# Kernel tuning notes

Hardware: AMD Instinct MI355X
Metric: run time of the kernel (lower is better)

Reference implementation:

```python
import jax, jax.numpy as jnp
import numpy as np

NTOKENS = 8192   # max_ntokens
TOPK = 2
H = 1024         # hidden
FFN = 4096       # ffn_hidden = 4*hidden
E = 8            # nexperts
M = NTOKENS * TOPK          # total dispatched rows (flux_m_max)
CAP = M // E                # balanced rows per expert


def setup_inputs() -> dict:
    key = jax.random.key(0)
    k1, k2, k3, k4 = jax.random.split(key, 4)
    x = jax.random.normal(k1, (NTOKENS, H), jnp.float32)
    weight0 = jax.random.normal(k2, (E, H, FFN), jnp.float32) * 0.02
    weight1 = jax.random.normal(k3, (E, FFN, H), jnp.float32) * 0.02
    # Balanced routing: scatter_index[t, k] is the row in the expert-sorted
    # dispatched buffer; a permutation of arange(M) gives exactly CAP rows/expert.
    scatter_index = jax.random.permutation(k4, M).reshape(NTOKENS, TOPK).astype(jnp.int32)
    splits = jnp.full((E,), CAP, dtype=jnp.int32)  # rows per expert, sum == M
    return {"x": x, "weight0": weight0, "weight1": weight1,
            "scatter_index": scatter_index, "splits": splits}


def reference(x, weight0, weight1, scatter_index, splits):
    ntokens, topk = scatter_index.shape
    n_exp, h, ffn = weight0.shape
    m = ntokens * topk
    cap = m // n_exp  # splits are balanced by construction (== splits[e])
    # --- AG-scatter: place each (token, k) replica at its dispatched row ---
    vals = jnp.repeat(x, topk, axis=0)                              # [M, h]
    dispatched = jnp.zeros((m, h), x.dtype).at[scatter_index.reshape(-1)].set(vals)
    xe = dispatched.reshape(n_exp, cap, h)                          # [E, C, h]
    # --- grouped GEMM 0 + exact GELU (torch F.gelu default = erf form) ---
    mid = jax.nn.gelu(jnp.einsum('ech,ehf->ecf', xe, weight0), approximate=False)
    # --- grouped GEMM 1 ---
    ye = jnp.einsum('ecf,efh->ech', mid, weight1).reshape(m, h)     # [M, h]
    # --- gather-RS: combine topk expert outputs per token ---
    return ye[scatter_index].sum(axis=1)                            # [ntokens, h]
```

## Files before the change

kernel.cpp:

```cpp
#include <hip/hip_runtime.h>
#include <hip/hip_bf16.h>
#include <cstdint>

constexpr int NT   = 8192;
constexpr int H    = 1024;
constexpr int FFN  = 4096;
constexpr int E    = 8;
constexpr int M    = NT * 2;
constexpr int CAP  = M / E;

typedef unsigned short u16;
typedef short short8 __attribute__((ext_vector_type(8)));
typedef float f32x4 __attribute__((ext_vector_type(4)));

__device__ int g_inv[M];

__device__ __forceinline__ u16 f2bf(float f) {
  union { float f; unsigned u; } c{f};
  unsigned r = (c.u + 0x7FFFu + ((c.u >> 16) & 1u)) >> 16;
  return (u16)r;
}
__device__ __forceinline__ void async16(const void* g, void* l) {
  auto gp = reinterpret_cast<const __attribute__((address_space(1))) unsigned*>(
      reinterpret_cast<uintptr_t>(g));
  auto lp = reinterpret_cast<__attribute__((address_space(3))) unsigned*>(
      reinterpret_cast<uintptr_t>(l));
  __builtin_amdgcn_global_load_lds(gp, lp, 16, 0, 0);
}

__device__ __forceinline__ void transpose_body(const float* __restrict__ W,
                                               u16* __restrict__ WT,
                                               int K, int N, int tb,
                                               void* smem_) {
  float (*tile)[65] = (float(*)[65])smem_;
  const int ntx = N >> 6;
  const int per = ntx * (K >> 6);
  const int e   = tb / per;
  const int rem = tb - e * per;
  const int bx  = rem % ntx;
  const int by  = rem / ntx;
  const float* Wp = W + (size_t)e * K * N;
  u16* Tp = WT + (size_t)e * K * N;
  const int k0 = by * 64, n0 = bx * 64;
  const int tid = threadIdx.x;

  const int u = tid & 15, krb = tid >> 4;
#pragma unroll
  for (int p = 0; p < 4; ++p) {
    const int kr = p * 16 + krb;
    float4 v = *(const float4*)&Wp[(size_t)(k0 + kr) * N + n0 + u * 4];
    tile[kr][u * 4 + 0] = v.x;
    tile[kr][u * 4 + 1] = v.y;
    tile[kr][u * 4 + 2] = v.z;
    tile[kr][u * 4 + 3] = v.w;
  }
  __syncthreads();

  const int n = tid >> 3, cb = tid & 7;
#pragma unroll
  for (int p = 0; p < 2; ++p) {
    const int nn = p * 32 + n;
    u16 pack[8];
#pragma unroll
    for (int j = 0; j < 8; ++j) pack[j] = f2bf(tile[cb * 8 + j][nn]);
    *(short8*)&Tp[(size_t)(n0 + nn) * K + k0 + cb * 8] = *(short8*)pack;
  }
}

__global__ __launch_bounds__(256)
void pre_kernel(const float* __restrict__ x, const float* __restrict__ w0,
                const int* __restrict__ sidx, u16* __restrict__ wt0,
                u16* __restrict__ disp, float* __restrict__ outz) {
  __shared__ float tile[64][65];
  const int b = blockIdx.x;
  const int tid = threadIdx.x;
  if (b < 8192) {
    transpose_body(w0, wt0, H, FFN, b, tile);
    return;
  }
  if (b < 16384) {
    const int t = b - 8192;
    const int r0 = sidx[2 * t + 0];
    const int r1 = sidx[2 * t + 1];
    float4 v = ((const float4*)(x + (size_t)t * H))[tid];
    ushort4 bb;
    bb.x = f2bf(v.x); bb.y = f2bf(v.y); bb.z = f2bf(v.z); bb.w = f2bf(v.w);
    ((ushort4*)disp)[(size_t)r0 * (H / 4) + tid] = bb;
    ((ushort4*)disp)[(size_t)r1 * (H / 4) + tid] = bb;
    return;
  }
  if (b < 16448) {
    const int i = (b - 16384) * 256 + tid;
    g_inv[sidx[i]] = i >> 1;
    return;
  }
  const int zb = b - 16448;
  float4 z = {0.f, 0.f, 0.f, 0.f};
#pragma unroll
  for (int p = 0; p < 4; ++p)
    ((float4*)outz)[(size_t)zb * 1024 + p * 256 + tid] = z;
}

template <bool GELU, bool ATOMIC>
__global__ __launch_bounds__(256)
void gemm_bt_kernel(const u16* __restrict__ A,
                    const u16* __restrict__ Bt,
                    u16* __restrict__ C,
                    float* __restrict__ outp,
                    int Mn, int Nn, int Kn, int ny,
                    const float* __restrict__ Wx, u16* __restrict__ WTx,
                    int Kx, int Nx) {
  __shared__ __align__(16) char smem[32768];
  int b = blockIdx.x;
  if (Wx != nullptr) {
    const int g = b / 3, r = b - g * 3;
    if (r != 0) { transpose_body(Wx, WTx, Kx, Nx, g * 2 + (r - 1), smem); return; }
    b = g;
  }
  u16* lA = (u16*)smem;
  u16* lB = (u16*)(smem + 16384);

  const int e = b & 7;
  const int t = b >> 3;
  const int q = t & 15, s = t >> 4;
  const int sy = ny >> 2;
  const int sm = s % sy, sn = s / sy;
  const int tm = sm * 4 + (q & 3), tn = sn * 4 + (q >> 2);
  const int m0 = tm * 128, n0 = tn * 128;

  const u16* Ae = A  + (size_t)e * Mn * Kn + (size_t)m0 * Kn;
  const u16* Be = Bt + (size_t)e * Nn * Kn + (size_t)n0 * Kn;

  const int tid  = threadIdx.x;
  const int lane = tid & 63;
  const int wave = tid >> 6;
  const int wr = wave >> 1, wc = wave & 1;
  const int lhi = lane >> 4, llo = lane & 15;

  const int sr = lane >> 3;
  const int gc = (lane & 7) ^ sr;

  f32x4 acc[4][4] = {};

  for (int kt = 0; kt < Kn; kt += 64) {
#pragma unroll
    for (int s2 = 0; s2 < 4; ++s2) {
      const int i = wave * 4 + s2;
      const int row = i * 8 + sr;
      async16(Ae + (size_t)row * Kn + kt + gc * 8, &lA[i * 512]);
      async16(Be + (size_t)row * Kn + kt + gc * 8, &lB[i * 512]);
    }
    __syncthreads();

#pragma unroll
    for (int ks = 0; ks < 2; ++ks) {
      short8 af[4], bf[4];
#pragma unroll
      for (int i = 0; i < 4; ++i) {
        const int row = wr * 64 + i * 16 + llo;
        const int pc = (ks * 4 + lhi) ^ (llo & 7);
        af[i] = *(const short8*)&lA[row * 64 + pc * 8];
      }
#pragma unroll
      for (int j = 0; j < 4; ++j) {
        const int row = wc * 64 + j * 16 + llo;
        const int pc = (ks * 4 + lhi) ^ (llo & 7);
        bf[j] = *(const short8*)&lB[row * 64 + pc * 8];
      }
#pragma unroll
      for (int i = 0; i < 4; ++i)
#pragma unroll
        for (int j = 0; j < 4; ++j)
          acc[i][j] = __builtin_amdgcn_mfma_f32_16x16x32_bf16(af[i], bf[j], acc[i][j], 0, 0, 0);
    }
    __syncthreads();
  }

  if (!ATOMIC) {
    u16* Ce = C + (size_t)e * Mn * Nn;
#pragma unroll
    for (int i = 0; i < 4; ++i) {
      const int mrow = m0 + wr * 64 + i * 16 + lhi * 4;
#pragma unroll
      for (int j = 0; j < 4; ++j) {
        const int ncol = n0 + wc * 64 + j * 16 + llo;
#pragma unroll
        for (int r = 0; r < 4; ++r) {
          float v = acc[i][j][r];
          if (GELU) v = 0.5f * v * (1.0f + erff(v * 0.70710678118654752f));
          Ce[(size_t)(mrow + r) * Nn + ncol] = f2bf(v);
        }
      }
    }
  } else {
    const int grBase = e * Mn + m0 + wr * 64;
#pragma unroll
    for (int i = 0; i < 4; ++i) {
      const int rb = grBase + i * 16 + lhi * 4;
#pragma unroll
      for (int r = 0; r < 4; ++r) {
        const int tok = g_inv[rb + r];
        float* orow = outp + (size_t)tok * H + n0 + wc * 64 + llo;
#pragma unroll
        for (int j = 0; j < 4; ++j)
          atomicAdd(orow + j * 16, acc[i][j][r]);
      }
    }
  }
}

__global__ __launch_bounds__(256)
void transpose_cvt_kernel(const float* __restrict__ W, u16* __restrict__ WT,
                          int K, int N) {
  __shared__ float tile[64][65];
  transpose_body(W, WT, K, N, blockIdx.x, tile);
}

extern "C" void kernel_launch(void* const* d_in, const int* in_sizes, int n_in,
                              void* d_out, int out_size, void* d_ws, size_t ws_size,
                              hipStream_t stream) {
  (void)in_sizes; (void)n_in; (void)out_size;
  const float* x    = (const float*)d_in[0];
  const float* w0   = (const float*)d_in[1];
  const float* w1   = (const float*)d_in[2];
  const int*   sidx = (const int*)d_in[3];
  float* out = (float*)d_out;

  char* ws = (char*)d_ws;
  const size_t MB = 1024ull * 1024;
  u16* wt0  = (u16*)ws;
  u16* disp = (u16*)(ws + 64 * MB);
  u16* mid  = (u16*)(ws + 96 * MB);
  const bool roomy = ws_size >= 288 * MB;
  u16* wt1 = roomy ? (u16*)(ws + 224 * MB) : wt0;

  pre_kernel<<<18496, 256, 0, stream>>>(x, w0, sidx, wt0, disp, out);

  if (roomy) {
    gemm_bt_kernel<true, false><<<12288, 256, 0, stream>>>(
        disp, wt0, mid, nullptr, CAP, FFN, H, CAP / 128, w1, wt1, FFN, H);
  } else {
    gemm_bt_kernel<true, false><<<4096, 256, 0, stream>>>(
        disp, wt0, mid, nullptr, CAP, FFN, H, CAP / 128, nullptr, nullptr, 0, 0);
    transpose_cvt_kernel<<<8192, 256, 0, stream>>>(w1, wt1, FFN, H);
  }

  gemm_bt_kernel<false, true><<<1024, 256, 0, stream>>>(
      mid, wt1, nullptr, out, CAP, H, FFN, CAP / 128, nullptr, nullptr, 0, 0);
}
```

Baseline: 730.3 us.

## Replace atomic combine with bf16 expert output plus gather-sum; fast GELU

The second grouped GEMM now writes bf16 per-expert outputs instead of scattering fp32 atomicAdds through an inverse index. A separate gather-sum kernel then adds the two top-k rows per token, which removes the output zeroing and the inverse-map construction. Both weight transposes move into the pre-kernel instead of being interleaved with GEMM0 blocks, and the token scatter is vectorized. Exact erf GELU is replaced with a sigmoid-style exp2 approximation, and the inner ks loop is no longer unrolled. This trades atomics for an extra bf16 round trip of the outputs, with some precision risk from the bf16 outputs and the approximate GELU.

Result: faster. 689.9 us (-5.5%).

```diff
diff --git a/kernel.cpp b/kernel.cpp
--- a/kernel.cpp
+++ b/kernel.cpp
@@ -13,12 +13,14 @@
 typedef short short8 __attribute__((ext_vector_type(8)));
 typedef float f32x4 __attribute__((ext_vector_type(4)));
 
-__device__ int g_inv[M];
-
 __device__ __forceinline__ u16 f2bf(float f) {
   union { float f; unsigned u; } c{f};
   unsigned r = (c.u + 0x7FFFu + ((c.u >> 16) & 1u)) >> 16;
   return (u16)r;
+}
+__device__ __forceinline__ float bf2f(u16 u) {
+  union { unsigned u; float f; } c{((unsigned)u) << 16};
+  return c.f;
 }
 __device__ __forceinline__ void async16(const void* g, void* l) {
   auto gp = reinterpret_cast<const __attribute__((address_space(1))) unsigned*>(
@@ -28,11 +30,16 @@
   __builtin_amdgcn_global_load_lds(gp, lp, 16, 0, 0);
 }
 
+__device__ __forceinline__ float gelu_fast(float x) {
+  const float u = x * x;
+  const float w = x * (-2.30220795f + -0.102943895f * u);
+  return x * __frcp_rn(1.0f + exp2f(w));
+}
+
 __device__ __forceinline__ void transpose_body(const float* __restrict__ W,
                                                u16* __restrict__ WT,
                                                int K, int N, int tb,
-                                               void* smem_) {
-  float (*tile)[65] = (float(*)[65])smem_;
+                                               float (*tile)[65]) {
   const int ntx = N >> 6;
   const int per = ntx * (K >> 6);
   const int e   = tb / per;
@@ -67,59 +74,56 @@
   }
 }
 
+__device__ __forceinline__ void scatter_body(const float* __restrict__ x,
+                                             const int* __restrict__ sidx,
+                                             u16* __restrict__ disp, int b) {
+  const int tid = threadIdx.x;
+  const int half = tid >> 7;
+  const int r = tid & 127;
+#pragma unroll
+  for (int it = 0; it < 2; ++it) {
+    const int t = it * 4096 + b * 2 + half;
+    const int r0 = sidx[2 * t + 0];
+    const int r1 = sidx[2 * t + 1];
+    const float4* xr = (const float4*)(x + (size_t)t * H);
+    float4 v0 = xr[r * 2 + 0];
+    float4 v1 = xr[r * 2 + 1];
+    u16 pk[8] = {f2bf(v0.x), f2bf(v0.y), f2bf(v0.z), f2bf(v0.w),
+                 f2bf(v1.x), f2bf(v1.y), f2bf(v1.z), f2bf(v1.w)};
+    *(short8*)&disp[(size_t)r0 * H + r * 8] = *(short8*)pk;
+    *(short8*)&disp[(size_t)r1 * H + r * 8] = *(short8*)pk;
+  }
+}
+
 __global__ __launch_bounds__(256)
 void pre_kernel(const float* __restrict__ x, const float* __restrict__ w0,
-                const int* __restrict__ sidx, u16* __restrict__ wt0,
-                u16* __restrict__ disp, float* __restrict__ outz) {
+                const float* __restrict__ w1, const int* __restrict__ sidx,
+                u16* __restrict__ wt0, u16* __restrict__ wt1,
+                u16* __restrict__ disp) {
   __shared__ float tile[64][65];
   const int b = blockIdx.x;
-  const int tid = threadIdx.x;
-  if (b < 8192) {
-    transpose_body(w0, wt0, H, FFN, b, tile);
-    return;
-  }
-  if (b < 16384) {
-    const int t = b - 8192;
-    const int r0 = sidx[2 * t + 0];
-    const int r1 = sidx[2 * t + 1];
-    float4 v = ((const float4*)(x + (size_t)t * H))[tid];
-    ushort4 bb;
-    bb.x = f2bf(v.x); bb.y = f2bf(v.y); bb.z = f2bf(v.z); bb.w = f2bf(v.w);
-    ((ushort4*)disp)[(size_t)r0 * (H / 4) + tid] = bb;
-    ((ushort4*)disp)[(size_t)r1 * (H / 4) + tid] = bb;
-    return;
-  }
-  if (b < 16448) {
-    const int i = (b - 16384) * 256 + tid;
-    g_inv[sidx[i]] = i >> 1;
-    return;
-  }
-  const int zb = b - 16448;
-  float4 z = {0.f, 0.f, 0.f, 0.f};
-#pragma unroll
-  for (int p = 0; p < 4; ++p)
-    ((float4*)outz)[(size_t)zb * 1024 + p * 256 + tid] = z;
-}
-
-template <bool GELU, bool ATOMIC>
+  if (b < 2048) { scatter_body(x, sidx, disp, b); return; }
+  if (b < 10240) { transpose_body(w0, wt0, H, FFN, b - 2048, tile); return; }
+  transpose_body(w1, wt1, FFN, H, b - 10240, tile);
+}
+
+__global__ __launch_bounds__(256)
+void transpose_cvt_kernel(const float* __restrict__ W, u16* __restrict__ WT,
+                          int K, int N) {
+  __shared__ float tile[64][65];
+  transpose_body(W, WT, K, N, blockIdx.x, tile);
+}
+
+template <bool GELU>
 __global__ __launch_bounds__(256)
 void gemm_bt_kernel(const u16* __restrict__ A,
                     const u16* __restrict__ Bt,
                     u16* __restrict__ C,
-                    float* __restrict__ outp,
-                    int Mn, int Nn, int Kn, int ny,
-                    const float* __restrict__ Wx, u16* __restrict__ WTx,
-                    int Kx, int Nx) {
-  __shared__ __align__(16) char smem[32768];
-  int b = blockIdx.x;
-  if (Wx != nullptr) {
-    const int g = b / 3, r = b - g * 3;
-    if (r != 0) { transpose_body(Wx, WTx, Kx, Nx, g * 2 + (r - 1), smem); return; }
-    b = g;
-  }
-  u16* lA = (u16*)smem;
-  u16* lB = (u16*)(smem + 16384);
-
+                    int Mn, int Nn, int Kn, int ny) {
+  __shared__ __align__(16) u16 lA[128 * 64];
+  __shared__ __align__(16) u16 lB[128 * 64];
+
+  const int b = blockIdx.x;
   const int e = b & 7;
   const int t = b >> 3;
   const int q = t & 15, s = t >> 4;
@@ -130,6 +134,7 @@
 
   const u16* Ae = A  + (size_t)e * Mn * Kn + (size_t)m0 * Kn;
   const u16* Be = Bt + (size_t)e * Nn * Kn + (size_t)n0 * Kn;
+  u16* Ce = C + (size_t)e * Mn * Nn;
 
   const int tid  = threadIdx.x;
   const int lane = tid & 63;
@@ -152,7 +157,7 @@
     }
     __syncthreads();
 
-#pragma unroll
+#pragma unroll 1
     for (int ks = 0; ks < 2; ++ks) {
       short8 af[4], bf[4];
 #pragma unroll
@@ -176,44 +181,49 @@
     __syncthreads();
   }
 
-  if (!ATOMIC) {
-    u16* Ce = C + (size_t)e * Mn * Nn;
-#pragma unroll
-    for (int i = 0; i < 4; ++i) {
-      const int mrow = m0 + wr * 64 + i * 16 + lhi * 4;
-#pragma unroll
-      for (int j = 0; j < 4; ++j) {
-        const int ncol = n0 + wc * 64 + j * 16 + llo;
-#pragma unroll
-        for (int r = 0; r < 4; ++r) {
-          float v = acc[i][j][r];
-          if (GELU) v = 0.5f * v * (1.0f + erff(v * 0.70710678118654752f));
-          Ce[(size_t)(mrow + r) * Nn + ncol] = f2bf(v);
-        }
+#pragma unroll
+  for (int i = 0; i < 4; ++i) {
+    const int mrow = m0 + wr * 64 + i * 16 + lhi * 4;
+#pragma unroll
+    for (int j = 0; j < 4; ++j) {
+      const int ncol = n0 + wc * 64 + j * 16 + llo;
+#pragma unroll
+      for (int r = 0; r < 4; ++r) {
+        float v = acc[i][j][r];
+        if (GELU) v = gelu_fast(v);
+        Ce[(size_t)(mrow + r) * Nn + ncol] = f2bf(v);
       }
     }
-  } else {
-    const int grBase = e * Mn + m0 + wr * 64;
-#pragma unroll
-    for (int i = 0; i < 4; ++i) {
-      const int rb = grBase + i * 16 + lhi * 4;
-#pragma unroll
-      for (int r = 0; r < 4; ++r) {
-        const int tok = g_inv[rb + r];
-        float* orow = outp + (size_t)tok * H + n0 + wc * 64 + llo;
-#pragma unroll
-        for (int j = 0; j < 4; ++j)
-          atomicAdd(orow + j * 16, acc[i][j][r]);
-      }
-    }
-  }
-}
-
-__global__ __launch_bounds__(256)
-void transpose_cvt_kernel(const float* __restrict__ W, u16* __restrict__ WT,
-                          int K, int N) {
-  __shared__ float tile[64][65];
-  transpose_body(W, WT, K, N, blockIdx.x, tile);
+  }
+}
+
+__global__ __launch_bounds__(256)
+void gather_sum_kernel(const u16* __restrict__ ye,
+                       const int* __restrict__ sidx,
+                       float* __restrict__ out) {
+  const int tid = threadIdx.x;
+  const int half = tid >> 7;
+  const int r = tid & 127;
+#pragma unroll
+  for (int it = 0; it < 2; ++it) {
+    const int t = it * 4096 + blockIdx.x * 2 + half;
+    const int r0 = sidx[2 * t + 0];
+    const int r1 = sidx[2 * t + 1];
+    short8 a = *(const short8*)&ye[(size_t)r0 * H + r * 8];
+    short8 b = *(const short8*)&ye[(size_t)r1 * H + r * 8];
+    float4 s0, s1;
+    s0.x = bf2f((u16)a[0]) + bf2f((u16)b[0]);
+    s0.y = bf2f((u16)a[1]) + bf2f((u16)b[1]);
+    s0.z = bf2f((u16)a[2]) + bf2f((u16)b[2]);
+    s0.w = bf2f((u16)a[3]) + bf2f((u16)b[3]);
+    s1.x = bf2f((u16)a[4]) + bf2f((u16)b[4]);
+    s1.y = bf2f((u16)a[5]) + bf2f((u16)b[5]);
+    s1.z = bf2f((u16)a[6]) + bf2f((u16)b[6]);
+    s1.w = bf2f((u16)a[7]) + bf2f((u16)b[7]);
+    float4* orow = (float4*)(out + (size_t)t * H);
+    orow[r * 2 + 0] = s0;
+    orow[r * 2 + 1] = s1;
+  }
 }
 
 extern "C" void kernel_launch(void* const* d_in, const int* in_sizes, int n_in,
@@ -229,22 +239,22 @@
   char* ws = (char*)d_ws;
   const size_t MB = 1024ull * 1024;
   u16* wt0  = (u16*)ws;
-  u16* disp = (u16*)(ws + 64 * MB);
-  u16* mid  = (u16*)(ws + 96 * MB);
+  u16* wt1  = (u16*)(ws + 64 * MB);
+  u16* disp = (u16*)(ws + 128 * MB);
+  u16* mid  = (u16*)(ws + 160 * MB);
+  u16* ye   = disp;
   const bool roomy = ws_size >= 288 * MB;
-  u16* wt1 = roomy ? (u16*)(ws + 224 * MB) : wt0;
-
-  pre_kernel<<<18496, 256, 0, stream>>>(x, w0, sidx, wt0, disp, out);
 
   if (roomy) {
-    gemm_bt_kernel<true, false><<<12288, 256, 0, stream>>>(
-        disp, wt0, mid, nullptr, CAP, FFN, H, CAP / 128, w1, wt1, FFN, H);
+    pre_kernel<<<18432, 256, 0, stream>>>(x, w0, w1, sidx, wt0, wt1, disp);
+    gemm_bt_kernel<true><<<4096, 256, 0, stream>>>(disp, wt0, mid, CAP, FFN, H, CAP / 128);
+    gemm_bt_kernel<false><<<1024, 256, 0, stream>>>(mid, wt1, ye, CAP, H, FFN, CAP / 128);
   } else {
-    gemm_bt_kernel<true, false><<<4096, 256, 0, stream>>>(
-        disp, wt0, mid, nullptr, CAP, FFN, H, CAP / 128, nullptr, nullptr, 0, 0);
+    wt1 = wt0;
+    pre_kernel<<<10240, 256, 0, stream>>>(x, w0, w1, sidx, wt0, wt1, disp);
+    gemm_bt_kernel<true><<<4096, 256, 0, stream>>>(disp, wt0, mid, CAP, FFN, H, CAP / 128);
     transpose_cvt_kernel<<<8192, 256, 0, stream>>>(w1, wt1, FFN, H);
-  }
-
-  gemm_bt_kernel<false, true><<<1024, 256, 0, stream>>>(
-      mid, wt1, nullptr, out, CAP, H, FFN, CAP / 128, nullptr, nullptr, 0, 0);
-}
+    gemm_bt_kernel<false><<<1024, 256, 0, stream>>>(mid, wt1, ye, CAP, H, FFN, CAP / 128);
+  }
+  gather_sum_kernel<<<2048, 256, 0, stream>>>(ye, sidx, out);
+}
```
